# Kernel tuning notes

Measured on AMD Instinct MI355X. Metric: run time of the kernel, lower is better.

Reference implementation:

```python
import jax, jax.numpy as jnp
import numpy as np

DIM = 1024
DIM_LATENT = 1024
DIM_HEAD = 64
INNER = max(DIM, DIM_LATENT)  # 1024
HEADS = INNER // DIM_HEAD     # 16
SCALE = DIM_HEAD ** -0.5
LN_EPS = 1e-5
RMS_EPS = 1e-8


def layernorm(x, g, b):
    mu = jnp.mean(x, axis=-1, keepdims=True)
    var = jnp.mean(jnp.square(x - mu), axis=-1, keepdims=True)
    return (x - mu) * jax.lax.rsqrt(var + LN_EPS) * g + b


def rmsnorm(x, gamma):
    # torch: x / clamp(norm(x,-1) * d**-0.5, eps) * gamma
    n = jnp.linalg.norm(x, axis=-1, keepdims=True) * (x.shape[-1] ** -0.5)
    return x / jnp.maximum(n, RMS_EPS) * gamma


def setup_inputs() -> dict:
    key = jax.random.key(0)
    ks = jax.random.split(key, 8)
    b, n, nl = 8, 2048, 512
    x = jax.random.normal(ks[0], (b, n, DIM), dtype=jnp.float32)
    latents = jax.random.normal(ks[1], (b, nl, DIM_LATENT), dtype=jnp.float32)
    mask = jax.random.randint(ks[2], (b, n), 0, 2).astype(bool)
    init = lambda k, shape, fan_in: jax.random.normal(k, shape, jnp.float32) * (fan_in ** -0.5)
    return {
        "x": x,
        "latents": latents,
        "mask": mask,
        "ln_x_g": jnp.ones((DIM,), jnp.float32),
        "ln_x_b": jnp.zeros((DIM,), jnp.float32),
        "ln_l_g": jnp.ones((DIM_LATENT,), jnp.float32),
        "ln_l_b": jnp.zeros((DIM_LATENT,), jnp.float32),
        "q_gamma": jnp.ones((DIM_HEAD,), jnp.float32),
        "k_gamma": jnp.ones((DIM_HEAD,), jnp.float32),
        "W_q": init(ks[3], (DIM_LATENT, INNER), DIM_LATENT),
        "W_kv": init(ks[4], (DIM, 2 * INNER), DIM),
        "W_out": init(ks[5], (INNER, DIM_LATENT), INNER),
        "b_out": jnp.zeros((DIM_LATENT,), jnp.float32),
    }


def reference(x, latents, mask, ln_x_g, ln_x_b, ln_l_g, ln_l_b,
              q_gamma, k_gamma, W_q, W_kv, W_out, b_out):
    b, n, _ = x.shape
    nl = latents.shape[1]
    xn = layernorm(x, ln_x_g, ln_x_b)
    ln = layernorm(latents, ln_l_g, ln_l_b)

    q = ln @ W_q                                   # [b, nl, inner]
    kv = jnp.concatenate([xn @ W_kv, ln @ W_kv], axis=1)  # [b, n+nl, 2*inner]
    k, v = kv[..., :INNER], kv[..., INNER:]

    to_heads = lambda t: t.reshape(t.shape[0], t.shape[1], HEADS, DIM_HEAD).transpose(0, 2, 1, 3)
    q, k, v = to_heads(q), to_heads(k), to_heads(v)  # [b, h, *, d]

    qn = rmsnorm(q, q_gamma) * SCALE
    kn = rmsnorm(k, k_gamma)

    sim = jnp.einsum('bhid,bhjd->bhij', qn, kn)      # [b, h, nl, n+nl]
    full_mask = jnp.pad(mask, ((0, 0), (0, nl)), constant_values=True)
    neg = -jnp.finfo(sim.dtype).max
    sim = jnp.where(full_mask[:, None, None, :], sim, neg)

    attn = jax.nn.softmax(sim.astype(jnp.float32), axis=-1).astype(sim.dtype)
    out = jnp.einsum('bhij,bhjd->bhid', attn, v)     # [b, h, nl, d]
    out = out.transpose(0, 2, 1, 3).reshape(b, nl, INNER)
    return out @ W_out + b_out
```

## Files before the change

### kernel.cpp

```cpp
#include <hip/hip_runtime.h>
#include <hip/hip_bf16.h>
#include <cfloat>
#include <cmath>

typedef __hip_bfloat16 bf16;
#define DEV_INLINE __device__ __forceinline__

typedef __attribute__((ext_vector_type(8))) short short8;
typedef __attribute__((ext_vector_type(4))) short short4v;
typedef __attribute__((ext_vector_type(4))) float float4v;

#define BATCH 8
#define NSEQ 2048
#define NLAT 512
#define DIM_ 1024
#define NKV 2560
#define HEADS_ 16
#define DHEAD 64
#define SCALE_ 0.125f
#define LN_EPS_ 1e-5f
#define RMS_EPS_ 1e-8f

DEV_INLINE float bf2f(bf16 v) { return __bfloat162float(v); }
DEV_INLINE bf16 f2bf(float v) { return __float2bfloat16(v); }
DEV_INLINE short bfbits(float x) { union { bf16 b; short s; } c; c.b = f2bf(x); return c.s; }

template<typename T> DEV_INLINE float ldf(const T* p);
template<> DEV_INLINE float ldf<float>(const float* p) { return *p; }
template<> DEV_INLINE float ldf<bf16>(const bf16* p)  { return __bfloat162float(*p); }

template<typename T> DEV_INLINE void stf(T* p, float v);
template<> DEV_INLINE void stf<float>(float* p, float v) { *p = v; }
template<> DEV_INLINE void stf<bf16>(bf16* p, float v)  { *p = __float2bfloat16(v); }

DEV_INLINE void gload16(const bf16* g, bf16* l) {
    __builtin_amdgcn_global_load_lds(
        (const __attribute__((address_space(1))) unsigned int*)g,
        (__attribute__((address_space(3))) unsigned int*)l,
        16, 0, 0);
}

__global__ void detect_kernel(const void* ones, int* flag) {
    unsigned w = *(const unsigned*)ones;
    flag[0] = (w == 0x3F803F80u) ? 1 : 0;
}

DEV_INLINE float block_sum_256(float v, float* sred) {
    #pragma unroll
    for (int o = 1; o < 64; o <<= 1) v += __shfl_xor(v, o, 64);
    int w = threadIdx.x >> 6;
    __syncthreads();
    if ((threadIdx.x & 63) == 0) sred[w] = v;
    __syncthreads();
    return sred[0] + sred[1] + sred[2] + sred[3];
}

template<typename T>
__global__ __launch_bounds__(256) void ln_all_kernel(
    const int* __restrict__ flag, int want,
    const T* __restrict__ x, const T* __restrict__ lat,
    const T* __restrict__ gx, const T* __restrict__ bx,
    const T* __restrict__ gl, const T* __restrict__ bl,
    bf16* __restrict__ out)
{
    if (flag[0] != want) return;
    __shared__ float sred[4];
    int r = blockIdx.x;
    const T* src; const T* g; const T* be; bf16* o;
    if (r < BATCH * NSEQ) {
        int b = r >> 11, i = r & 2047;
        src = x + (size_t)r * DIM_;
        o = out + ((size_t)b * NKV + i) * DIM_;
        g = gx; be = bx;
    } else {
        int rr = r - BATCH * NSEQ;
        int b = rr >> 9, i = rr & 511;
        src = lat + (size_t)rr * DIM_;
        o = out + ((size_t)b * NKV + NSEQ + i) * DIM_;
        g = gl; be = bl;
    }
    int t = threadIdx.x;

    float v[4];
    float s = 0.f;
    #pragma unroll
    for (int j = 0; j < 4; j++) { v[j] = ldf(src + t + j * 256); s += v[j]; }
    s = block_sum_256(s, sred);
    float mu = s * (1.f / 1024.f);
    float s2 = 0.f;
    #pragma unroll
    for (int j = 0; j < 4; j++) { float d = v[j] - mu; s2 += d * d; }
    s2 = block_sum_256(s2, sred);
    float rstd = rsqrtf(s2 * (1.f / 1024.f) + LN_EPS_);
    #pragma unroll
    for (int j = 0; j < 4; j++) {
        int c = t + j * 256;
        o[c] = f2bf((v[j] - mu) * rstd * ldf(g + c) + ldf(be + c));
    }
}

template<typename T>
__global__ __launch_bounds__(256) void transpose_all_kernel(
    const int* __restrict__ flag, int want,
    const T* __restrict__ wq, const T* __restrict__ wkv, const T* __restrict__ wout,
    bf16* __restrict__ wqT, bf16* __restrict__ wkvT, bf16* __restrict__ woutT)
{
    if (flag[0] != want) return;
    __shared__ float tile[32][33];
    int bid = blockIdx.x;
    const T* in; bf16* out; int N, t0;
    if (bid < 1024)      { in = wq;   out = wqT;   N = 1024; t0 = bid; }
    else if (bid < 3072) { in = wkv;  out = wkvT;  N = 2048; t0 = bid - 1024; }
    else                 { in = wout; out = woutT; N = 1024; t0 = bid - 3072; }
    int K = 1024;
    int nb = N >> 5;
    int bn = (t0 % nb) * 32, bk = (t0 / nb) * 32;
    int tx = threadIdx.x & 31, ty = threadIdx.x >> 5;
    #pragma unroll
    for (int j = 0; j < 4; j++)
        tile[ty + j * 8][tx] = ldf(in + (size_t)(bk + ty + j * 8) * N + bn + tx);
    __syncthreads();
    #pragma unroll
    for (int j = 0; j < 4; j++)
        out[(size_t)(bn + ty + j * 8) * K + bk + tx] = f2bf(tile[tx][ty + j * 8]);
}

template<typename TC, int MODE, int RMS>
__global__ __launch_bounds__(256) void gemm_mfma(
    const int* __restrict__ flag, int want,
    const bf16* __restrict__ A, const bf16* __restrict__ Bt,
    const TC* __restrict__ bias, TC* __restrict__ C,
    const bf16* __restrict__ gamma_b, const float* __restrict__ gamma_f,
    int N, int K)
{
    int f = flag[0];
    if (want >= 0 && f != want) return;
    __shared__ bf16 As[128 * 64];
    __shared__ bf16 Bs[128 * 64];

    int tid = threadIdx.x;
    int bn = blockIdx.x, bm = blockIdx.y;
    int wv = tid >> 6, lane = tid & 63, quad = lane >> 4, l16 = lane & 15;
    int wm = wv >> 1, wn = wv & 1;

    const bf16* Apt[4]; const bf16* Bpt[4];
    #pragma unroll
    for (int rep = 0; rep < 4; rep++) {
        int c = rep * 256 + tid;
        int row = c >> 3;
        int k8 = ((c & 7) ^ (row & 7)) * 8;
        int ar = bm * 128 + row;
        int am = (MODE == 1) ? ((ar >> 9) * NKV + NSEQ + (ar & 511)) : ar;
        Apt[rep] = A + (size_t)am * K + k8;
        Bpt[rep] = Bt + (size_t)(bn * 128 + row) * K + k8;
    }
    bf16* Asl = &As[tid * 8];
    bf16* Bsl = &Bs[tid * 8];

    float4v acc[4][4];
    #pragma unroll
    for (int i = 0; i < 4; i++)
        #pragma unroll
        for (int j = 0; j < 4; j++)
            #pragma unroll
            for (int r = 0; r < 4; r++) acc[i][j][r] = 0.f;

    for (int k0 = 0; k0 < K; k0 += 64) {
        __syncthreads();
        #pragma unroll
        for (int rep = 0; rep < 4; rep++) {
            gload16(Apt[rep] + k0, Asl + rep * 2048);
            gload16(Bpt[rep] + k0, Bsl + rep * 2048);
        }
        __syncthreads();

        #pragma unroll
        for (int kk = 0; kk < 2; kk++) {
            short8 af[4], bfr[4];
            #pragma unroll
            for (int ms = 0; ms < 4; ms++) {
                int row = wm * 64 + ms * 16 + l16;
                int jc = (kk * 4 + quad) ^ (row & 7);
                af[ms] = *(const short8*)&As[row * 64 + jc * 8];
            }
            #pragma unroll
            for (int ns = 0; ns < 4; ns++) {
                int row = wn * 64 + ns * 16 + l16;
                int jc = (kk * 4 + quad) ^ (row & 7);
                bfr[ns] = *(const short8*)&Bs[row * 64 + jc * 8];
            }
            #pragma unroll
            for (int ms = 0; ms < 4; ms++)
                #pragma unroll
                for (int ns = 0; ns < 4; ns++)
                    acc[ms][ns] = __builtin_amdgcn_mfma_f32_16x16x32_bf16(af[ms], bfr[ns], acc[ms][ns], 0, 0, 0);
        }
    }

    if (RMS != 0) {
        bool dorms = (RMS == 2) || (bn * 256 < N);
        if (dorms) {
            float g4[4];
            #pragma unroll
            for (int ns = 0; ns < 4; ns++) {
                int idx = ns * 16 + l16;
                g4[ns] = f ? bf2f(gamma_b[idx]) : gamma_f[idx];
            }
            #pragma unroll
            for (int ms = 0; ms < 4; ms++) {
                #pragma unroll
                for (int r = 0; r < 4; r++) {
                    float ss = 0.f;
                    #pragma unroll
                    for (int ns = 0; ns < 4; ns++) ss += acc[ms][ns][r] * acc[ms][ns][r];
                    ss += __shfl_xor(ss, 1, 64);
                    ss += __shfl_xor(ss, 2, 64);
                    ss += __shfl_xor(ss, 4, 64);
                    ss += __shfl_xor(ss, 8, 64);
                    float n = sqrtf(ss) * 0.125f;
                    float inv = 1.0f / fmaxf(n, RMS_EPS_);
                    if (RMS == 2) inv *= SCALE_;
                    #pragma unroll
                    for (int ns = 0; ns < 4; ns++) acc[ms][ns][r] *= inv * g4[ns];
                }
            }
        }
    }

    #pragma unroll
    for (int ms = 0; ms < 4; ms++) {
        int row0 = bm * 128 + wm * 64 + ms * 16 + quad * 4;
        #pragma unroll
        for (int ns = 0; ns < 4; ns++) {
            int col = bn * 128 + wn * 64 + ns * 16 + l16;
            float bv = bias ? ldf(bias + col) : 0.f;
            TC* cp = C + (size_t)row0 * N + col;
            #pragma unroll
            for (int r = 0; r < 4; r++)
                stf(cp + (size_t)r * N, acc[ms][ns][r] + bv);
        }
    }
}

#define KC 64
__global__ __launch_bounds__(256) void attn_mfma(
    const bf16* __restrict__ q, const bf16* __restrict__ kv,
    const int* __restrict__ maskp, bf16* __restrict__ out)
{
    __shared__ bf16 Ks[KC][72];
    __shared__ bf16 Vt[DHEAD][72];
    __shared__ bf16 Ps[4][2][16][72];
    __shared__ float msk_s[KC];

    int tid = threadIdx.x;
    int bid = blockIdx.x;
    int bh = bid & 127, qb = bid >> 7;
    int h = bh & 15, bb = bh >> 4;
    int wv = tid >> 6, lane = tid & 63, quad = lane >> 4, l16 = lane & 15;
    int q8 = quad * 8;
    int qbase = qb * 128 + wv * 32;

    short8 qf[2][2];
    #pragma unroll
    for (int qt = 0; qt < 2; qt++) {
        const bf16* qp = q + ((size_t)(bb * NLAT + qbase + qt * 16 + l16)) * 1024 + h * DHEAD;
        qf[qt][0] = *(const short8*)(qp + q8);
        qf[qt][1] = *(const short8*)(qp + q8 + 32);
    }

    float4v o_acc[2][4];
    #pragma unroll
    for (int qt = 0; qt < 2; qt++)
        #pragma unroll
        for (int ds = 0; ds < 4; ds++)
            #pragma unroll
            for (int r = 0; r < 4; r++) o_acc[qt][ds][r] = 0.f;
    float m_i[2] = {-3.0e38f, -3.0e38f}, l_i[2] = {0.f, 0.f};

    for (int kb = 0; kb < NKV; kb += KC) {
        __syncthreads();
        #pragma unroll
        for (int rep = 0; rep < 2; rep++) {
            int p = tid + rep * 256;
            int key = p >> 3, du8 = (p & 7) * 8;
            uint4 kvv = *(const uint4*)(kv + ((size_t)(bb * NKV + kb + key)) * 2048 + h * DHEAD + du8);
            *(uint4*)&Ks[key][du8] = kvv;
        }
        {
            int kp = tid >> 3, du8 = (tid & 7) * 8;
            int key = kp * 2;
            const bf16* vp = kv + ((size_t)(bb * NKV + kb + key)) * 2048 + 1024 + h * DHEAD + du8;
            uint4 v0 = *(const uint4*)vp;
            uint4 v1 = *(const uint4*)(vp + 2048);
            const unsigned short* a0 = (const unsigned short*)&v0;
            const unsigned short* a1 = (const unsigned short*)&v1;
            #pragma unroll
            for (int j = 0; j < 8; j++) {
                unsigned pack = (unsigned)a0[j] | ((unsigned)a1[j] << 16);
                *(unsigned*)&Vt[du8 + j][key] = pack;
            }
        }
        if (tid < KC) {
            int key = kb + tid;
            float mv = 0.f;
            if (key < NSEQ) mv = maskp[bb * NSEQ + key] ? 0.f : -1e30f;
            msk_s[tid] = mv;
        }
        __syncthreads();

        float4v st[2][4];
        #pragma unroll
        for (int kt = 0; kt < 4; kt++) {
            short8 kf0 = *(const short8*)&Ks[kt * 16 + l16][q8];
            short8 kf1 = *(const short8*)&Ks[kt * 16 + l16][q8 + 32];
            #pragma unroll
            for (int qt = 0; qt < 2; qt++) {
                float4v z; z[0]=0.f; z[1]=0.f; z[2]=0.f; z[3]=0.f;
                z = __builtin_amdgcn_mfma_f32_16x16x32_bf16(kf0, qf[qt][0], z, 0, 0, 0);
                z = __builtin_amdgcn_mfma_f32_16x16x32_bf16(kf1, qf[qt][1], z, 0, 0, 0);
                st[qt][kt] = z;
            }
        }
        float4 mv4[4];
        #pragma unroll
        for (int kt = 0; kt < 4; kt++) mv4[kt] = *(const float4*)&msk_s[kt * 16 + 4 * quad];
        #pragma unroll
        for (int qt = 0; qt < 2; qt++) {
            float cmax = -3.0e38f;
            #pragma unroll
            for (int kt = 0; kt < 4; kt++) {
                const float* mk = (const float*)&mv4[kt];
                #pragma unroll
                for (int r = 0; r < 4; r++) {
                    float v = st[qt][kt][r] + mk[r];
                    st[qt][kt][r] = v;
                    cmax = fmaxf(cmax, v);
                }
            }
            cmax = fmaxf(cmax, __shfl_xor(cmax, 16, 64));
            cmax = fmaxf(cmax, __shfl_xor(cmax, 32, 64));
            float m_new = fmaxf(m_i[qt], cmax);
            float alpha = __expf(m_i[qt] - m_new);

            float psum = 0.f;
            #pragma unroll
            for (int kt = 0; kt < 4; kt++) {
                short4v pk;
                #pragma unroll
                for (int r = 0; r < 4; r++) {
                    float e = __expf(st[qt][kt][r] - m_new);
                    psum += e;
                    pk[r] = bfbits(e);
                }
                *(short4v*)&Ps[wv][qt][l16][kt * 16 + 4 * quad] = pk;
            }
            psum += __shfl_xor(psum, 16, 64);
            psum += __shfl_xor(psum, 32, 64);
            l_i[qt] = l_i[qt] * alpha + psum;
            m_i[qt] = m_new;
            #pragma unroll
            for (int ds = 0; ds < 4; ds++)
                #pragma unroll
                for (int r = 0; r < 4; r++) o_acc[qt][ds][r] *= alpha;
        }

        #pragma unroll
        for (int kc = 0; kc < 2; kc++) {
            short8 pf[2];
            #pragma unroll
            for (int qt = 0; qt < 2; qt++)
                pf[qt] = *(const short8*)&Ps[wv][qt][l16][kc * 32 + q8];
            #pragma unroll
            for (int ds = 0; ds < 4; ds++) {
                short8 vf = *(const short8*)&Vt[ds * 16 + l16][kc * 32 + q8];
                #pragma unroll
                for (int qt = 0; qt < 2; qt++)
                    o_acc[qt][ds] = __builtin_amdgcn_mfma_f32_16x16x32_bf16(vf, pf[qt], o_acc[qt][ds], 0, 0, 0);
            }
        }
    }

    #pragma unroll
    for (int qt = 0; qt < 2; qt++) {
        float inv = 1.0f / l_i[qt];
        bf16* op = out + ((size_t)(bb * NLAT + qbase + qt * 16 + l16)) * 1024 + h * DHEAD;
        #pragma unroll
        for (int ds = 0; ds < 4; ds++) {
            short4v ov;
            #pragma unroll
            for (int r = 0; r < 4; r++) ov[r] = bfbits(o_acc[qt][ds][r] * inv);
            *(short4v*)(op + ds * 16 + 4 * quad) = ov;
        }
    }
}

extern "C" void kernel_launch(void* const* d_in, const int* in_sizes, int n_in,
                              void* d_out, int out_size, void* d_ws, size_t ws_size,
                              hipStream_t stream) {
    const int* mask = (const int*)d_in[2];

    char* ws = (char*)d_ws;
    size_t off = 0;
    int*  flag    = (int*)(ws + off);  off += 256;
    bf16* cat_n   = (bf16*)(ws + off); off += (size_t)20480 * 1024 * 2;
    bf16* kvbuf   = (bf16*)(ws + off); off += (size_t)20480 * 2048 * 2;
    bf16* qbuf    = (bf16*)(ws + off); off += (size_t)4096 * 1024 * 2;
    bf16* attnout = (bf16*)(ws + off); off += (size_t)4096 * 1024 * 2;
    bf16* wqT     = (bf16*)(ws + off); off += (size_t)1024 * 1024 * 2;
    bf16* wkvT    = (bf16*)(ws + off); off += (size_t)2048 * 1024 * 2;
    bf16* woutT   = (bf16*)(ws + off); off += (size_t)1024 * 1024 * 2;

    detect_kernel<<<1, 1, 0, stream>>>(d_in[3], flag);

    ln_all_kernel<bf16><<<BATCH*NSEQ + BATCH*NLAT, 256, 0, stream>>>(flag, 1,
        (const bf16*)d_in[0], (const bf16*)d_in[1],
        (const bf16*)d_in[3], (const bf16*)d_in[4],
        (const bf16*)d_in[5], (const bf16*)d_in[6], cat_n);
    ln_all_kernel<float><<<BATCH*NSEQ + BATCH*NLAT, 256, 0, stream>>>(flag, 0,
        (const float*)d_in[0], (const float*)d_in[1],
        (const float*)d_in[3], (const float*)d_in[4],
        (const float*)d_in[5], (const float*)d_in[6], cat_n);

    transpose_all_kernel<bf16><<<4096, 256, 0, stream>>>(flag, 1,
        (const bf16*)d_in[9], (const bf16*)d_in[10], (const bf16*)d_in[11],
        wqT, wkvT, woutT);
    transpose_all_kernel<float><<<4096, 256, 0, stream>>>(flag, 0,
        (const float*)d_in[9], (const float*)d_in[10], (const float*)d_in[11],
        wqT, wkvT, woutT);

    gemm_mfma<bf16, 0, 1><<<dim3(2048/128, 20480/128), 256, 0, stream>>>(flag, -1,
        cat_n, wkvT, (const bf16*)nullptr, kvbuf,
        (const bf16*)d_in[8], (const float*)d_in[8], 2048, 1024);

    gemm_mfma<bf16, 1, 2><<<dim3(1024/128, 4096/128), 256, 0, stream>>>(flag, -1,
        cat_n, wqT, (const bf16*)nullptr, qbuf,
        (const bf16*)d_in[7], (const float*)d_in[7], 1024, 1024);

    attn_mfma<<<dim3(512), 256, 0, stream>>>(qbuf, kvbuf, mask, attnout);

    gemm_mfma<bf16, 0, 0><<<dim3(1024/128, 4096/128), 256, 0, stream>>>(flag, 1,
        attnout, woutT, (const bf16*)d_in[12], (bf16*)d_out,
        (const bf16*)nullptr, (const float*)nullptr, 1024, 1024);
    gemm_mfma<float, 0, 0><<<dim3(1024/128, 4096/128), 256, 0, stream>>>(flag, 0,
        attnout, woutT, (const float*)d_in[12], (float*)d_out,
        (const bf16*)nullptr, (const float*)nullptr, 1024, 1024);
}
```

Measured before the change: 413.6 us.

## Write V transposed from KV GEMM epilogue and async-load swizzled K/V tiles in attention

The KV projection GEMM now splits its output: K goes to a dense [tokens,1024] buffer and V is written pre-transposed per (batch, head, d) along keys. The attention kernel then loads K and V tiles straight into XOR-swizzled shared memory with gload16, with no per-iteration register transpose of V. This removes the shuffle/pack work and the strided 2048-wide reads in the attention inner loop. In exchange the GEMM epilogue does scattered 8-byte transposed stores. gload16 is assumed to be a helper defined in the part of the file not shown.

```diff
diff --git a/kernel.cpp b/kernel.cpp
--- a/kernel.cpp
+++ b/kernel.cpp
@@ -129,7 +129,7 @@
 __global__ __launch_bounds__(256) void gemm_mfma(
     const int* __restrict__ flag, int want,
     const bf16* __restrict__ A, const bf16* __restrict__ Bt,
-    const TC* __restrict__ bias, TC* __restrict__ C,
+    const TC* __restrict__ bias, TC* __restrict__ C, bf16* __restrict__ VT,
     const bf16* __restrict__ gamma_b, const float* __restrict__ gamma_f,
     int N, int K)
 {
@@ -198,7 +198,7 @@
     }
 
     if (RMS != 0) {
-        bool dorms = (RMS == 2) || (bn * 256 < N);
+        bool dorms = (RMS == 2) || (bn < 8);
         if (dorms) {
             float g4[4];
             #pragma unroll
@@ -227,28 +227,48 @@
         }
     }
 
-    #pragma unroll
-    for (int ms = 0; ms < 4; ms++) {
-        int row0 = bm * 128 + wm * 64 + ms * 16 + quad * 4;
-        #pragma unroll
-        for (int ns = 0; ns < 4; ns++) {
-            int col = bn * 128 + wn * 64 + ns * 16 + l16;
-            float bv = bias ? ldf(bias + col) : 0.f;
-            TC* cp = C + (size_t)row0 * N + col;
-            #pragma unroll
-            for (int r = 0; r < 4; r++)
-                stf(cp + (size_t)r * N, acc[ms][ns][r] + bv);
+    if (RMS == 1 && bn >= 8) {
+        int bq = bm / 20;
+        int keyb = (bm % 20) * 128 + wm * 64;
+        #pragma unroll
+        for (int ms = 0; ms < 4; ms++) {
+            int key = keyb + ms * 16 + quad * 4;
+            #pragma unroll
+            for (int ns = 0; ns < 4; ns++) {
+                int col = bn * 128 + wn * 64 + ns * 16 + l16 - 1024;
+                int h = col >> 6, d = col & 63;
+                short4v ov;
+                #pragma unroll
+                for (int r = 0; r < 4; r++) ov[r] = bfbits(acc[ms][ns][r]);
+                *(short4v*)(VT + ((size_t)((bq * 16 + h) * 64 + d)) * NKV + key) = ov;
+            }
+        }
+    } else {
+        int NC = (RMS == 1) ? 1024 : N;
+        #pragma unroll
+        for (int ms = 0; ms < 4; ms++) {
+            int row0 = bm * 128 + wm * 64 + ms * 16 + quad * 4;
+            #pragma unroll
+            for (int ns = 0; ns < 4; ns++) {
+                int col = bn * 128 + wn * 64 + ns * 16 + l16;
+                float bv = bias ? ldf(bias + col) : 0.f;
+                TC* cp = C + (size_t)row0 * NC + col;
+                #pragma unroll
+                for (int r = 0; r < 4; r++)
+                    stf(cp + (size_t)r * NC, acc[ms][ns][r] + bv);
+            }
         }
     }
 }
 
 #define KC 64
 __global__ __launch_bounds__(256) void attn_mfma(
-    const bf16* __restrict__ q, const bf16* __restrict__ kv,
+    const bf16* __restrict__ q, const bf16* __restrict__ kbuf,
+    const bf16* __restrict__ vtbuf,
     const int* __restrict__ maskp, bf16* __restrict__ out)
 {
-    __shared__ bf16 Ks[KC][72];
-    __shared__ bf16 Vt[DHEAD][72];
+    __shared__ bf16 Ks[KC * 64];
+    __shared__ bf16 Vt[DHEAD * 64];
     __shared__ bf16 Ps[4][2][16][72];
     __shared__ float msk_s[KC];
 
@@ -260,6 +280,9 @@
     int q8 = quad * 8;
     int qbase = qb * 128 + wv * 32;
 
+    const bf16* kbase = kbuf + (size_t)bb * NKV * 1024 + h * DHEAD;
+    const bf16* vbase = vtbuf + (size_t)(bb * 16 + h) * DHEAD * NKV;
+
     short8 qf[2][2];
     #pragma unroll
     for (int qt = 0; qt < 2; qt++) {
@@ -268,6 +291,10 @@
         qf[qt][1] = *(const short8*)(qp + q8 + 32);
     }
 
+    int c0 = tid, c1 = tid + 256;
+    int krow0 = c0 >> 3, kj0 = ((c0 & 7) ^ (krow0 & 7)) * 8;
+    int krow1 = c1 >> 3, kj1 = ((c1 & 7) ^ (krow1 & 7)) * 8;
+
     float4v o_acc[2][4];
     #pragma unroll
     for (int qt = 0; qt < 2; qt++)
@@ -279,27 +306,10 @@
 
     for (int kb = 0; kb < NKV; kb += KC) {
         __syncthreads();
-        #pragma unroll
-        for (int rep = 0; rep < 2; rep++) {
-            int p = tid + rep * 256;
-            int key = p >> 3, du8 = (p & 7) * 8;
-            uint4 kvv = *(const uint4*)(kv + ((size_t)(bb * NKV + kb + key)) * 2048 + h * DHEAD + du8);
-            *(uint4*)&Ks[key][du8] = kvv;
-        }
-        {
-            int kp = tid >> 3, du8 = (tid & 7) * 8;
-            int key = kp * 2;
-            const bf16* vp = kv + ((size_t)(bb * NKV + kb + key)) * 2048 + 1024 + h * DHEAD + du8;
-            uint4 v0 = *(const uint4*)vp;
-            uint4 v1 = *(const uint4*)(vp + 2048);
-            const unsigned short* a0 = (const unsigned short*)&v0;
-            const unsigned short* a1 = (const unsigned short*)&v1;
-            #pragma unroll
-            for (int j = 0; j < 8; j++) {
-                unsigned pack = (unsigned)a0[j] | ((unsigned)a1[j] << 16);
-                *(unsigned*)&Vt[du8 + j][key] = pack;
-            }
-        }
+        gload16(kbase + (size_t)(kb + krow0) * 1024 + kj0, &Ks[c0 * 8]);
+        gload16(kbase + (size_t)(kb + krow1) * 1024 + kj1, &Ks[c1 * 8]);
+        gload16(vbase + (size_t)krow0 * NKV + kb + kj0, &Vt[c0 * 8]);
+        gload16(vbase + (size_t)krow1 * NKV + kb + kj1, &Vt[c1 * 8]);
         if (tid < KC) {
             int key = kb + tid;
             float mv = 0.f;
@@ -311,8 +321,9 @@
         float4v st[2][4];
         #pragma unroll
         for (int kt = 0; kt < 4; kt++) {
-            short8 kf0 = *(const short8*)&Ks[kt * 16 + l16][q8];
-            short8 kf1 = *(const short8*)&Ks[kt * 16 + l16][q8 + 32];
+            int row = kt * 16 + l16;
+            short8 kf0 = *(const short8*)&Ks[row * 64 + ((quad ^ (l16 & 7)) << 3)];
+            short8 kf1 = *(const short8*)&Ks[row * 64 + (((quad + 4) ^ (l16 & 7)) << 3)];
             #pragma unroll
             for (int qt = 0; qt < 2; qt++) {
                 float4v z; z[0]=0.f; z[1]=0.f; z[2]=0.f; z[3]=0.f;
@@ -372,7 +383,8 @@
                 pf[qt] = *(const short8*)&Ps[wv][qt][l16][kc * 32 + q8];
             #pragma unroll
             for (int ds = 0; ds < 4; ds++) {
-                short8 vf = *(const short8*)&Vt[ds * 16 + l16][kc * 32 + q8];
+                int row = ds * 16 + l16;
+                short8 vf = *(const short8*)&Vt[row * 64 + (((kc * 4 + quad) ^ (l16 & 7)) << 3)];
                 #pragma unroll
                 for (int qt = 0; qt < 2; qt++)
                     o_acc[qt][ds] = __builtin_amdgcn_mfma_f32_16x16x32_bf16(vf, pf[qt], o_acc[qt][ds], 0, 0, 0);
@@ -403,7 +415,8 @@
     size_t off = 0;
     int*  flag    = (int*)(ws + off);  off += 256;
     bf16* cat_n   = (bf16*)(ws + off); off += (size_t)20480 * 1024 * 2;
-    bf16* kvbuf   = (bf16*)(ws + off); off += (size_t)20480 * 2048 * 2;
+    bf16* kbuf    = (bf16*)(ws + off); off += (size_t)20480 * 1024 * 2;
+    bf16* vtbuf   = (bf16*)(ws + off); off += (size_t)8192 * 2560 * 2;
     bf16* qbuf    = (bf16*)(ws + off); off += (size_t)4096 * 1024 * 2;
     bf16* attnout = (bf16*)(ws + off); off += (size_t)4096 * 1024 * 2;
     bf16* wqT     = (bf16*)(ws + off); off += (size_t)1024 * 1024 * 2;
@@ -429,19 +442,19 @@
         wqT, wkvT, woutT);
 
     gemm_mfma<bf16, 0, 1><<<dim3(2048/128, 20480/128), 256, 0, stream>>>(flag, -1,
-        cat_n, wkvT, (const bf16*)nullptr, kvbuf,
+        cat_n, wkvT, (const bf16*)nullptr, kbuf, vtbuf,
         (const bf16*)d_in[8], (const float*)d_in[8], 2048, 1024);
 
     gemm_mfma<bf16, 1, 2><<<dim3(1024/128, 4096/128), 256, 0, stream>>>(flag, -1,
-        cat_n, wqT, (const bf16*)nullptr, qbuf,
+        cat_n, wqT, (const bf16*)nullptr, qbuf, (bf16*)nullptr,
         (const bf16*)d_in[7], (const float*)d_in[7], 1024, 1024);
 
-    attn_mfma<<<dim3(512), 256, 0, stream>>>(qbuf, kvbuf, mask, attnout);
+    attn_mfma<<<dim3(512), 256, 0, stream>>>(qbuf, kbuf, vtbuf, mask, attnout);
 
     gemm_mfma<bf16, 0, 0><<<dim3(1024/128, 4096/128), 256, 0, stream>>>(flag, 1,
-        attnout, woutT, (const bf16*)d_in[12], (bf16*)d_out,
+        attnout, woutT, (const bf16*)d_in[12], (bf16*)d_out, (bf16*)nullptr,
         (const bf16*)nullptr, (const float*)nullptr, 1024, 1024);
     gemm_mfma<float, 0, 0><<<dim3(1024/128, 4096/128), 256, 0, stream>>>(flag, 0,
-        attnout, woutT, (const float*)d_in[12], (float*)d_out,
+        attnout, woutT, (const float*)d_in[12], (float*)d_out, (bf16*)nullptr,
         (const bf16*)nullptr, (const float*)nullptr, 1024, 1024);
 }
```

Result: faster. 400.2 us (-3.3%).
